# Optimization experiments

Hardware: AMD Instinct MI355X
Metric: run time of the kernel (lower is better)

Reference implementation:

```python
import jax, jax.numpy as jnp
import numpy as np

N = 50000          # nodes
E = 1200000        # edges (before self loops)
HID = 256          # hidden_dim
HEADS = 4
DH = HID // HEADS  # head dim = 64
SLOPE = 0.2        # PyG GATConv default negative_slope


def setup_inputs() -> dict:
    key = jax.random.key(0)
    k1, k2, k3, k4, k5 = jax.random.split(key, 5)
    x = jax.random.normal(k1, (N, HID), dtype=jnp.float32)
    # GATConv params: shared linear W, per-head attention vectors a_src/a_dst, bias
    W = jax.random.normal(k2, (HID, HEADS * DH), dtype=jnp.float32) / np.float32(np.sqrt(HID))
    att_src = jax.random.normal(k3, (HEADS, DH), dtype=jnp.float32) * 0.1
    att_dst = jax.random.normal(k4, (HEADS, DH), dtype=jnp.float32) * 0.1
    bias = jnp.zeros((HEADS * DH,), dtype=jnp.float32)
    edge_index = jax.random.randint(k5, (2, E), 0, N, dtype=jnp.int32)
    return {"x": x, "W": W, "att_src": att_src, "att_dst": att_dst,
            "bias": bias, "edge_index": edge_index}


def reference(x, W, att_src, att_dst, bias, edge_index):
    # add self loops (PyG GATConv default add_self_loops=True)
    loops = jnp.arange(N, dtype=edge_index.dtype)
    src = jnp.concatenate([edge_index[0], loops])  # message source
    dst = jnpp_dst = jnp.concatenate([edge_index[1], loops])  # message target / softmax segment

    h = (x @ W).reshape(N, HEADS, DH)                       # [N,H,D]
    a_s = jnp.einsum('nhd,hd->nh', h, att_src)              # [N,H]
    a_d = jnp.einsum('nhd,hd->nh', h, att_dst)              # [N,H]

    e = jax.nn.leaky_relu(a_s[src] + a_d[dst], SLOPE)       # [Etot,H] edge logits
    # segment-wise (per destination node) stable softmax
    emax = jax.ops.segment_max(e, dst, num_segments=N)      # [N,H]
    ez = jnp.exp(e - emax[dst])
    denom = jax.ops.segment_sum(ez, dst, num_segments=N)    # [N,H]
    alpha = ez / (denom[dst] + 1e-16)                       # [Etot,H]

    msg = h[src] * alpha[:, :, None]                        # [Etot,H,D]
    out = jax.ops.segment_sum(msg, dst, num_segments=N)     # [N,H,D]
    out = out.reshape(N, HEADS * DH) + bias                 # concat heads + bias
    return jax.nn.relu(out)
```

## Files before the change

### kernel.cpp

```cpp
#include <hip/hip_runtime.h>
#include <hip/hip_bf16.h>
#include <hip/hip_fp16.h>

#define HID 256
#define HEADS 4
#define DH 64
#define SLOPE 0.2f
#define NBMAX 512
#define BCAP 4096

typedef __attribute__((ext_vector_type(8))) _Float16 f16x8;
typedef __attribute__((ext_vector_type(4))) float f32x4;

__device__ inline float leaky(float x) { return x >= 0.f ? x : SLOPE * x; }

__global__ __launch_bounds__(256) void transpose_w(const float* __restrict__ W,
                                                   _Float16* __restrict__ Wt,
                                                   int* __restrict__ bucket_cursor) {
  int n = blockIdx.x;
  int k = threadIdx.x;
  Wt[n * HID + k] = (_Float16)W[(size_t)k * HID + n];
  if (n == 0) {
    bucket_cursor[k] = 0;
    bucket_cursor[k + 256] = 0;
  }
}

__global__ __launch_bounds__(256) void fused_gemm_scatter(
    const float* __restrict__ X, const _Float16* __restrict__ Wt,
    const float* __restrict__ att_src, const float* __restrict__ att_dst,
    _Float16* __restrict__ Hp, float* __restrict__ as4, float* __restrict__ ad4,
    const int* __restrict__ ei, int E, int Etot,
    int* __restrict__ bucket_cursor, unsigned* __restrict__ tmp,
    int NB, int nbEdge, int M) {
  __shared__ __align__(16) char smem[20480];
  const int t = threadIdx.x;

  if ((int)blockIdx.x < nbEdge) {
    int* h = (int*)smem;
    int* cur = h + NBMAX;
    for (int i = t; i < NB; i += 256) h[i] = 0;
    __syncthreads();
    const int g0 = blockIdx.x * 1024;
#pragma unroll
    for (int j = 0; j < 4; ++j) {
      const int e0 = (g0 + j * 256 + t) * 4;
      if (e0 >= Etot) continue;
      if (e0 >= E) {
#pragma unroll
        for (int k = 0; k < 4; ++k) atomicAdd(&h[(e0 - E + k) >> 7], 1);
      } else {
        const int4 d4 = *(const int4*)(ei + E + e0);
        atomicAdd(&h[d4.x >> 7], 1);
        atomicAdd(&h[d4.y >> 7], 1);
        atomicAdd(&h[d4.z >> 7], 1);
        atomicAdd(&h[d4.w >> 7], 1);
      }
    }
    __syncthreads();
    for (int i = t; i < NB; i += 256)
      cur[i] = h[i] ? (i * BCAP + atomicAdd(&bucket_cursor[i], h[i])) : 0;
    __syncthreads();
#pragma unroll
    for (int j = 0; j < 4; ++j) {
      const int e0 = (g0 + j * 256 + t) * 4;
      if (e0 >= Etot) continue;
      int s[4], dn[4];
      if (e0 >= E) {
#pragma unroll
        for (int k = 0; k < 4; ++k) { s[k] = e0 - E + k; dn[k] = s[k]; }
      } else {
        const int4 s4 = *(const int4*)(ei + e0);
        const int4 d4 = *(const int4*)(ei + E + e0);
        s[0] = s4.x; s[1] = s4.y; s[2] = s4.z; s[3] = s4.w;
        dn[0] = d4.x; dn[1] = d4.y; dn[2] = d4.z; dn[3] = d4.w;
      }
#pragma unroll
      for (int k = 0; k < 4; ++k) {
        const int b = dn[k] >> 7;
        const int pos = atomicAdd(&cur[b], 1);
        tmp[pos] = (unsigned)s[k] | ((unsigned)(dn[k] & 127) << 16);
      }
    }
    return;
  }

  _Float16 (*sA)[32][40] = (_Float16 (*)[32][40])smem;
  const int head = t >> 6;
  const int l = t & 63;
  const int lr = l & 15;
  const int lk = l >> 4;
  const int row0 = ((int)blockIdx.x - nbEdge) * 32;

  {
    const int r = t >> 3;
    const int ksb = t & 7;
    const int gr = row0 + r;
    _Float16 tmpv[32];
    if (gr < M) {
      const float* p = X + (size_t)gr * HID + ksb * 32;
#pragma unroll
      for (int j = 0; j < 8; ++j) {
        const float4 v = *(const float4*)(p + j * 4);
        tmpv[j * 4 + 0] = (_Float16)v.x;
        tmpv[j * 4 + 1] = (_Float16)v.y;
        tmpv[j * 4 + 2] = (_Float16)v.z;
        tmpv[j * 4 + 3] = (_Float16)v.w;
      }
    } else {
#pragma unroll
      for (int j = 0; j < 32; ++j) tmpv[j] = (_Float16)0.f;
    }
#pragma unroll
    for (int j = 0; j < 4; ++j)
      *(uint4*)&sA[ksb][r][j * 8] = *(const uint4*)&tmpv[j * 8];
  }
  __syncthreads();

  f32x4 acc[2][4] = {};
#pragma unroll
  for (int ks = 0; ks < 8; ++ks) {
    f16x8 af[2];
#pragma unroll
    for (int mt = 0; mt < 2; ++mt)
      af[mt] = *(const f16x8*)&sA[ks][mt * 16 + lr][lk * 8];
#pragma unroll
    for (int nt = 0; nt < 4; ++nt) {
      const f16x8 bfr = *(const f16x8*)(Wt + (size_t)(head * 64 + nt * 16 + lr) * HID
                                        + ks * 32 + lk * 8);
#pragma unroll
      for (int mt = 0; mt < 2; ++mt)
        acc[mt][nt] = __builtin_amdgcn_mfma_f32_16x16x32_f16(af[mt], bfr, acc[mt][nt], 0, 0, 0);
    }
  }

  float as_v[4], ad_v[4];
#pragma unroll
  for (int nt = 0; nt < 4; ++nt) {
    as_v[nt] = att_src[head * DH + nt * 16 + lr];
    ad_v[nt] = att_dst[head * DH + nt * 16 + lr];
  }
#pragma unroll
  for (int mt = 0; mt < 2; ++mt) {
#pragma unroll
    for (int reg = 0; reg < 4; ++reg) {
      float ps = 0.f, pd = 0.f;
#pragma unroll
      for (int nt = 0; nt < 4; ++nt) {
        ps += acc[mt][nt][reg] * as_v[nt];
        pd += acc[mt][nt][reg] * ad_v[nt];
      }
#pragma unroll
      for (int off = 1; off < 16; off <<= 1) {
        ps += __shfl_xor(ps, off, 64);
        pd += __shfl_xor(pd, off, 64);
      }
      const int row = row0 + mt * 16 + lk * 4 + reg;
      if (lr == 0 && row < M) {
        as4[(size_t)row * 4 + head] = ps;
        ad4[(size_t)row * 4 + head] = pd;
      }
    }
  }

#pragma unroll
  for (int mt = 0; mt < 2; ++mt) {
#pragma unroll
    for (int nt = 0; nt < 4; ++nt) {
      const int dh = nt * 16 + lr;
#pragma unroll
      for (int reg = 0; reg < 4; ++reg) {
        const int row = row0 + mt * 16 + lk * 4 + reg;
        if (row < M)
          Hp[((size_t)head * M + row) * DH + dh] = (_Float16)acc[mt][nt][reg];
      }
    }
  }
}

__global__ __launch_bounds__(256) void csr_build(const unsigned* __restrict__ tmp,
                                                 const int* __restrict__ bucket_cursor,
                                                 int* __restrict__ starts,
                                                 int* __restrict__ ends,
                                                 unsigned* __restrict__ csr_h,
                                                 const float4* __restrict__ as4,
                                                 const float4* __restrict__ ad4,
                                                 int Nn, int csrStride) {
  __shared__ int h[128], cur[128];
  __shared__ unsigned cs[BCAP];
  const int b = blockIdx.x;
  const int base = b * BCAP;
  const int cnt = min(bucket_cursor[b], BCAP);
  const int tid = threadIdx.x;
  if (tid < 128) h[tid] = 0;
  __syncthreads();
  for (int i = tid; i < cnt; i += 256)
    atomicAdd(&h[tmp[base + i] >> 16], 1);
  __syncthreads();
  const int own = (tid < 128) ? h[tid] : 0;
#pragma unroll
  for (int off = 1; off < 128; off <<= 1) {
    const int t = (tid < 128 && tid >= off) ? h[tid - off] : 0;
    __syncthreads();
    if (tid < 128) h[tid] += t;
    __syncthreads();
  }
  if (tid < 128) {
    const int excl = h[tid] - own;
    cur[tid] = excl;
    const int n = b * 128 + tid;
    if (n < Nn) {
      starts[n] = base + excl;
      ends[n] = base + excl + own;
    }
  }
  __syncthreads();
  for (int i = tid; i < cnt; i += 256) {
    const unsigned p = tmp[base + i];
    const int pos = atomicAdd(&cur[p >> 16], 1);
    cs[pos] = p;
  }
  __syncthreads();
  for (int i = tid; i < cnt; i += 256) {
    const unsigned pe = cs[i];
    const int src = (int)(pe & 0xffffu);
    const int dnl = (int)(pe >> 16);
    const float4 a = as4[src];
    const float4 d = ad4[b * 128 + dnl];
    const float p0 = __expf(leaky(a.x + d.x));
    const float p1 = __expf(leaky(a.y + d.y));
    const float p2 = __expf(leaky(a.z + d.z));
    const float p3 = __expf(leaky(a.w + d.w));
    csr_h[base + i] = (unsigned)src |
                      ((unsigned)__half_as_ushort(__float2half(p0)) << 16);
    csr_h[csrStride + base + i] = (unsigned)src |
                      ((unsigned)__half_as_ushort(__float2half(p1)) << 16);
    csr_h[2 * csrStride + base + i] = (unsigned)src |
                      ((unsigned)__half_as_ushort(__float2half(p2)) << 16);
    csr_h[3 * csrStride + base + i] = (unsigned)src |
                      ((unsigned)__half_as_ushort(__float2half(p3)) << 16);
  }
}

__global__ __launch_bounds__(256) void gat_agg2(const int* __restrict__ starts,
                                                const int* __restrict__ ends,
                                                const unsigned* __restrict__ csr_h,
                                                const _Float16* __restrict__ Hp,
                                                const float* __restrict__ bias,
                                                float* __restrict__ out,
                                                int Nn, int nbNode, int csrStride) {
  const int head = blockIdx.x / nbNode;
  const int nb   = blockIdx.x - head * nbNode;
  const int wave = threadIdx.x >> 6;
  const int lane = threadIdx.x & 63;
  const int half = lane >> 5;
  const int hl   = lane & 31;
  const int g2   = hl >> 3;
  const int sl   = hl & 7;
  const int n    = nb * 8 + wave * 2 + half;

  int start = 0, end = 0;
  if (n < Nn) { start = starts[n]; end = ends[n]; }
  const unsigned* __restrict__ ch = csr_h + (size_t)head * csrStride;
  const _Float16* __restrict__ Hh = Hp + (size_t)head * Nn * DH + sl * 8;

  float lpart = 0.f;
  __half2 acc[4];
#pragma unroll
  for (int j = 0; j < 4; ++j) acc[j] = __float2half2_rn(0.f);

  const int nChunk = (end - start + 31) >> 5;
  for (int c = 0; c < nChunk; ++c) {
    const int base = start + c * 32;
    const int cnt = min(32, end - base);
    const int idx = min(base + hl, end - 1);
    const unsigned ce = ch[idx];
    const bool valid = hl < cnt;
    const unsigned combo = valid ? ce : (ce & 0xffffu);
    lpart += valid ? __half2float(__ushort_as_half((unsigned short)(ce >> 16))) : 0.f;

    const int nIt = (cnt + 3) >> 2;
#pragma unroll 4
    for (int i = 0; i < nIt; ++i) {
      const int e = i * 4 + g2;
      const unsigned cc = (unsigned)__shfl((int)combo, half * 32 + e, 64);
      const unsigned se = cc & 0xffffu;
      const __half ah = __ushort_as_half((unsigned short)(cc >> 16));
      const __half2 a2 = __halves2half2(ah, ah);
      const uint4 hv = *(const uint4*)(Hh + (size_t)se * DH);
      acc[0] = __hfma2(a2, *(const __half2*)&hv.x, acc[0]);
      acc[1] = __hfma2(a2, *(const __half2*)&hv.y, acc[1]);
      acc[2] = __hfma2(a2, *(const __half2*)&hv.z, acc[2]);
      acc[3] = __hfma2(a2, *(const __half2*)&hv.w, acc[3]);
    }
  }
#pragma unroll
  for (int off = 16; off > 0; off >>= 1) lpart += __shfl_xor(lpart, off, 64);
#pragma unroll
  for (int off = 8; off <= 16; off <<= 1)
#pragma unroll
    for (int j = 0; j < 4; ++j) {
      int tbits = __shfl_xor(*(const int*)&acc[j], off, 64);
      acc[j] = __hadd2(acc[j], *(const __half2*)&tbits);
    }

  if (hl < 8 && n < Nn) {
    const float inv = 1.f / (lpart + 1e-16f);
    float v[8];
#pragma unroll
    for (int j = 0; j < 4; ++j) {
      v[2 * j]     = __low2float(acc[j]);
      v[2 * j + 1] = __high2float(acc[j]);
    }
#pragma unroll
    for (int j = 0; j < 8; ++j)
      v[j] = fmaxf(v[j] * inv + bias[head * DH + sl * 8 + j], 0.f);
    float* op = out + (size_t)n * HID + head * DH + sl * 8;
    *(float4*)op = make_float4(v[0], v[1], v[2], v[3]);
    *(float4*)(op + 4) = make_float4(v[4], v[5], v[6], v[7]);
  }
}

extern "C" void kernel_launch(void* const* d_in, const int* in_sizes, int n_in,
                              void* d_out, int out_size, void* d_ws, size_t ws_size,
                              hipStream_t stream) {
  const float* x       = (const float*)d_in[0];
  const float* Wm      = (const float*)d_in[1];
  const float* att_src = (const float*)d_in[2];
  const float* att_dst = (const float*)d_in[3];
  const float* bias    = (const float*)d_in[4];
  const int*   ei      = (const int*)d_in[5];

  const int Nn   = in_sizes[0] / HID;
  const int E    = in_sizes[5] / 2;
  const int Etot = E + Nn;
  const int NB   = (Nn + 127) >> 7;
  const int csrStride = NB * BCAP;

  float* out = (float*)d_out;

  _Float16* Hp    = (_Float16*)d_ws;
  _Float16* Wt    = Hp + (size_t)HEADS * Nn * DH;
  float* as4      = (float*)(Wt + HID * HID);
  float* ad4      = as4 + (size_t)Nn * 4;
  int*   starts   = (int*)(ad4 + (size_t)Nn * 4);
  int*   ends     = starts + Nn;
  int*   bucket_cursor = ends + Nn;
  unsigned* tmp   = (unsigned*)(bucket_cursor + NBMAX);
  unsigned* csr_h = tmp + (size_t)csrStride;

  const int nbNode = (Nn + 7) / 8;
  const int nbEdge = (Etot + 4095) / 4096;
  const int nbGemm = (Nn + 31) / 32;

  transpose_w<<<HID, HID, 0, stream>>>(Wm, Wt, bucket_cursor);
  fused_gemm_scatter<<<nbEdge + nbGemm, 256, 0, stream>>>(
      x, Wt, att_src, att_dst, Hp, as4, ad4,
      ei, E, Etot, bucket_cursor, tmp, NB, nbEdge, Nn);
  csr_build<<<NB, 256, 0, stream>>>(tmp, bucket_cursor, starts, ends, csr_h,
                                    (const float4*)as4, (const float4*)ad4,
                                    Nn, csrStride);
  gat_agg2<<<HEADS * nbNode, 256, 0, stream>>>(starts, ends, csr_h,
                                               Hp, bias, out, Nn, nbNode, csrStride);
}
```

Before: 146.7 us.

## Fuse CSR build into per-bucket aggregation, keeping CSR in shared memory

The CSR construction kernel and the aggregation kernel are merged into one kernel with one block per (head, 128-node bucket). The block sorts its bucket's edges by destination in LDS, computes per-head exp logits in place, then aggregates its nodes directly from shared memory. This removes one launch and the global write and re-read of the four per-head CSR arrays and the start/end arrays. In exchange, the histogram and sort work is repeated once per head, and there are fewer, heavier blocks (4×NB ≈ 1564), each looping serially over 128 nodes, which may cause load imbalance.

```diff
diff --git a/kernel.cpp b/kernel.cpp
--- a/kernel.cpp
+++ b/kernel.cpp
@@ -178,21 +178,30 @@
   }
 }
 
-__global__ __launch_bounds__(256) void csr_build(const unsigned* __restrict__ tmp,
-                                                 const int* __restrict__ bucket_cursor,
-                                                 int* __restrict__ starts,
-                                                 int* __restrict__ ends,
-                                                 unsigned* __restrict__ csr_h,
-                                                 const float4* __restrict__ as4,
-                                                 const float4* __restrict__ ad4,
-                                                 int Nn, int csrStride) {
+__global__ __launch_bounds__(256) void gat_bucket_agg(
+    const unsigned* __restrict__ tmp,
+    const int* __restrict__ bucket_cursor,
+    const float* __restrict__ as4,
+    const float* __restrict__ ad4,
+    const _Float16* __restrict__ Hp,
+    const float* __restrict__ bias,
+    float* __restrict__ out, int Nn, int NB) {
+  __shared__ unsigned cs[BCAP];
   __shared__ int h[128], cur[128];
-  __shared__ unsigned cs[BCAP];
-  const int b = blockIdx.x;
+  __shared__ int starts_l[128], cnts_l[128];
+  __shared__ float ad_l[128];
+
+  const int head = blockIdx.x / NB;
+  const int b    = blockIdx.x - head * NB;
+  const int tid  = threadIdx.x;
   const int base = b * BCAP;
-  const int cnt = min(bucket_cursor[b], BCAP);
-  const int tid = threadIdx.x;
-  if (tid < 128) h[tid] = 0;
+  const int cnt  = min(bucket_cursor[b], BCAP);
+
+  if (tid < 128) {
+    const int n = b * 128 + tid;
+    ad_l[tid] = (n < Nn) ? ad4[(size_t)n * 4 + head] : 0.f;
+    h[tid] = 0;
+  }
   __syncthreads();
   for (int i = tid; i < cnt; i += 256)
     atomicAdd(&h[tmp[base + i] >> 16], 1);
@@ -208,116 +217,94 @@
   if (tid < 128) {
     const int excl = h[tid] - own;
     cur[tid] = excl;
-    const int n = b * 128 + tid;
-    if (n < Nn) {
-      starts[n] = base + excl;
-      ends[n] = base + excl + own;
-    }
+    starts_l[tid] = excl;
+    cnts_l[tid] = own;
   }
   __syncthreads();
   for (int i = tid; i < cnt; i += 256) {
-    const unsigned p = tmp[base + i];
-    const int pos = atomicAdd(&cur[p >> 16], 1);
-    cs[pos] = p;
+    const unsigned pe = tmp[base + i];
+    const int pos = atomicAdd(&cur[pe >> 16], 1);
+    cs[pos] = pe;
   }
   __syncthreads();
   for (int i = tid; i < cnt; i += 256) {
     const unsigned pe = cs[i];
     const int src = (int)(pe & 0xffffu);
     const int dnl = (int)(pe >> 16);
-    const float4 a = as4[src];
-    const float4 d = ad4[b * 128 + dnl];
-    const float p0 = __expf(leaky(a.x + d.x));
-    const float p1 = __expf(leaky(a.y + d.y));
-    const float p2 = __expf(leaky(a.z + d.z));
-    const float p3 = __expf(leaky(a.w + d.w));
-    csr_h[base + i] = (unsigned)src |
-                      ((unsigned)__half_as_ushort(__float2half(p0)) << 16);
-    csr_h[csrStride + base + i] = (unsigned)src |
-                      ((unsigned)__half_as_ushort(__float2half(p1)) << 16);
-    csr_h[2 * csrStride + base + i] = (unsigned)src |
-                      ((unsigned)__half_as_ushort(__float2half(p2)) << 16);
-    csr_h[3 * csrStride + base + i] = (unsigned)src |
-                      ((unsigned)__half_as_ushort(__float2half(p3)) << 16);
-  }
-}
-
-__global__ __launch_bounds__(256) void gat_agg2(const int* __restrict__ starts,
-                                                const int* __restrict__ ends,
-                                                const unsigned* __restrict__ csr_h,
-                                                const _Float16* __restrict__ Hp,
-                                                const float* __restrict__ bias,
-                                                float* __restrict__ out,
-                                                int Nn, int nbNode, int csrStride) {
-  const int head = blockIdx.x / nbNode;
-  const int nb   = blockIdx.x - head * nbNode;
-  const int wave = threadIdx.x >> 6;
-  const int lane = threadIdx.x & 63;
+    const float p = __expf(leaky(as4[(size_t)src * 4 + head] + ad_l[dnl]));
+    cs[i] = (unsigned)src | ((unsigned)__half_as_ushort(__float2half(p)) << 16);
+  }
+  __syncthreads();
+
+  const int wave = tid >> 6;
+  const int lane = tid & 63;
   const int half = lane >> 5;
   const int hl   = lane & 31;
   const int g2   = hl >> 3;
   const int sl   = hl & 7;
-  const int n    = nb * 8 + wave * 2 + half;
-
-  int start = 0, end = 0;
-  if (n < Nn) { start = starts[n]; end = ends[n]; }
-  const unsigned* __restrict__ ch = csr_h + (size_t)head * csrStride;
   const _Float16* __restrict__ Hh = Hp + (size_t)head * Nn * DH + sl * 8;
 
-  float lpart = 0.f;
-  __half2 acc[4];
-#pragma unroll
-  for (int j = 0; j < 4; ++j) acc[j] = __float2half2_rn(0.f);
-
-  const int nChunk = (end - start + 31) >> 5;
-  for (int c = 0; c < nChunk; ++c) {
-    const int base = start + c * 32;
-    const int cnt = min(32, end - base);
-    const int idx = min(base + hl, end - 1);
-    const unsigned ce = ch[idx];
-    const bool valid = hl < cnt;
-    const unsigned combo = valid ? ce : (ce & 0xffffu);
-    lpart += valid ? __half2float(__ushort_as_half((unsigned short)(ce >> 16))) : 0.f;
-
-    const int nIt = (cnt + 3) >> 2;
+  for (int it = 0; it < 16; ++it) {
+    const int slot = it * 8 + wave * 2 + half;
+    const int start = starts_l[slot];
+    const int ccnt  = cnts_l[slot];
+    const int n = b * 128 + slot;
+
+    float lpart = 0.f;
+    __half2 acc[4];
+#pragma unroll
+    for (int j = 0; j < 4; ++j) acc[j] = __float2half2_rn(0.f);
+
+    const int nChunk = (ccnt + 31) >> 5;
+    for (int c = 0; c < nChunk; ++c) {
+      const int cb = start + c * 32;
+      const int rem = min(32, start + ccnt - cb);
+      const int idx = min(cb + hl, start + ccnt - 1);
+      const unsigned ce = cs[idx];
+      const bool valid = hl < rem;
+      const unsigned combo = valid ? ce : (ce & 0xffffu);
+      lpart += valid ? __half2float(__ushort_as_half((unsigned short)(ce >> 16))) : 0.f;
+
+      const int nIt = (rem + 3) >> 2;
 #pragma unroll 4
-    for (int i = 0; i < nIt; ++i) {
-      const int e = i * 4 + g2;
-      const unsigned cc = (unsigned)__shfl((int)combo, half * 32 + e, 64);
-      const unsigned se = cc & 0xffffu;
-      const __half ah = __ushort_as_half((unsigned short)(cc >> 16));
-      const __half2 a2 = __halves2half2(ah, ah);
-      const uint4 hv = *(const uint4*)(Hh + (size_t)se * DH);
-      acc[0] = __hfma2(a2, *(const __half2*)&hv.x, acc[0]);
-      acc[1] = __hfma2(a2, *(const __half2*)&hv.y, acc[1]);
-      acc[2] = __hfma2(a2, *(const __half2*)&hv.z, acc[2]);
-      acc[3] = __hfma2(a2, *(const __half2*)&hv.w, acc[3]);
-    }
-  }
-#pragma unroll
-  for (int off = 16; off > 0; off >>= 1) lpart += __shfl_xor(lpart, off, 64);
-#pragma unroll
-  for (int off = 8; off <= 16; off <<= 1)
-#pragma unroll
-    for (int j = 0; j < 4; ++j) {
-      int tbits = __shfl_xor(*(const int*)&acc[j], off, 64);
-      acc[j] = __hadd2(acc[j], *(const __half2*)&tbits);
-    }
-
-  if (hl < 8 && n < Nn) {
-    const float inv = 1.f / (lpart + 1e-16f);
-    float v[8];
-#pragma unroll
-    for (int j = 0; j < 4; ++j) {
-      v[2 * j]     = __low2float(acc[j]);
-      v[2 * j + 1] = __high2float(acc[j]);
-    }
-#pragma unroll
-    for (int j = 0; j < 8; ++j)
-      v[j] = fmaxf(v[j] * inv + bias[head * DH + sl * 8 + j], 0.f);
-    float* op = out + (size_t)n * HID + head * DH + sl * 8;
-    *(float4*)op = make_float4(v[0], v[1], v[2], v[3]);
-    *(float4*)(op + 4) = make_float4(v[4], v[5], v[6], v[7]);
+      for (int i = 0; i < nIt; ++i) {
+        const int e = i * 4 + g2;
+        const unsigned cc = (unsigned)__shfl((int)combo, half * 32 + e, 64);
+        const unsigned se = cc & 0xffffu;
+        const __half ah = __ushort_as_half((unsigned short)(cc >> 16));
+        const __half2 a2 = __halves2half2(ah, ah);
+        const uint4 hv = *(const uint4*)(Hh + (size_t)se * DH);
+        acc[0] = __hfma2(a2, *(const __half2*)&hv.x, acc[0]);
+        acc[1] = __hfma2(a2, *(const __half2*)&hv.y, acc[1]);
+        acc[2] = __hfma2(a2, *(const __half2*)&hv.z, acc[2]);
+        acc[3] = __hfma2(a2, *(const __half2*)&hv.w, acc[3]);
+      }
+    }
+#pragma unroll
+    for (int off = 16; off > 0; off >>= 1) lpart += __shfl_xor(lpart, off, 64);
+#pragma unroll
+    for (int off = 8; off <= 16; off <<= 1)
+#pragma unroll
+      for (int j = 0; j < 4; ++j) {
+        int tbits = __shfl_xor(*(const int*)&acc[j], off, 64);
+        acc[j] = __hadd2(acc[j], *(const __half2*)&tbits);
+      }
+
+    if (hl < 8 && n < Nn) {
+      const float inv = 1.f / (lpart + 1e-16f);
+      float v[8];
+#pragma unroll
+      for (int j = 0; j < 4; ++j) {
+        v[2 * j]     = __low2float(acc[j]);
+        v[2 * j + 1] = __high2float(acc[j]);
+      }
+#pragma unroll
+      for (int j = 0; j < 8; ++j)
+        v[j] = fmaxf(v[j] * inv + bias[head * DH + sl * 8 + j], 0.f);
+      float* op = out + (size_t)n * HID + head * DH + sl * 8;
+      *(float4*)op = make_float4(v[0], v[1], v[2], v[3]);
+      *(float4*)(op + 4) = make_float4(v[4], v[5], v[6], v[7]);
+    }
   }
 }
 
@@ -335,7 +322,6 @@
   const int E    = in_sizes[5] / 2;
   const int Etot = E + Nn;
   const int NB   = (Nn + 127) >> 7;
-  const int csrStride = NB * BCAP;
 
   float* out = (float*)d_out;
 
@@ -343,13 +329,9 @@
   _Float16* Wt    = Hp + (size_t)HEADS * Nn * DH;
   float* as4      = (float*)(Wt + HID * HID);
   float* ad4      = as4 + (size_t)Nn * 4;
-  int*   starts   = (int*)(ad4 + (size_t)Nn * 4);
-  int*   ends     = starts + Nn;
-  int*   bucket_cursor = ends + Nn;
+  int*   bucket_cursor = (int*)(ad4 + (size_t)Nn * 4);
   unsigned* tmp   = (unsigned*)(bucket_cursor + NBMAX);
-  unsigned* csr_h = tmp + (size_t)csrStride;
-
-  const int nbNode = (Nn + 7) / 8;
+
   const int nbEdge = (Etot + 4095) / 4096;
   const int nbGemm = (Nn + 31) / 32;
 
@@ -357,9 +339,6 @@
   fused_gemm_scatter<<<nbEdge + nbGemm, 256, 0, stream>>>(
       x, Wt, att_src, att_dst, Hp, as4, ad4,
       ei, E, Etot, bucket_cursor, tmp, NB, nbEdge, Nn);
-  csr_build<<<NB, 256, 0, stream>>>(tmp, bucket_cursor, starts, ends, csr_h,
-                                    (const float4*)as4, (const float4*)ad4,
-                                    Nn, csrStride);
-  gat_agg2<<<HEADS * nbNode, 256, 0, stream>>>(starts, ends, csr_h,
-                                               Hp, bias, out, Nn, nbNode, csrStride);
+  gat_bucket_agg<<<HEADS * NB, 256, 0, stream>>>(tmp, bucket_cursor, as4, ad4,
+                                                 Hp, bias, out, Nn, NB);
 }
```

After: 174.1 us. 18.6% more time.
